# Performance work log

Hardware: AMD Instinct MI355X
Metric: run time of the kernel (lower is better)

The kernel has to match this reference:

```python
import jax, jax.numpy as jnp
import numpy as np
from jax import lax

B, C, H, W = 4, 192, 64, 64
D_STATE, D_CONV, EXPAND = 16, 4, 2.0
DI = int(EXPAND * C)           # 384 inner dim
DT_RANK = (C + 15) // 16       # 12
EPS = 1e-5


def setup_inputs() -> dict:
    key = jax.random.key(0)
    ks = jax.random.split(key, 16)
    r = lambda k, shp, s=0.02: jax.random.normal(k, shp, jnp.float32) * s
    inp = {
        'x': jax.random.normal(ks[0], (B, C, H, W), jnp.float32),
        'ln_w': jnp.ones((C,), jnp.float32),
        'ln_b': jnp.zeros((C,), jnp.float32),
        'in_proj_w': r(ks[1], (2 * DI, C)),
        'conv_w': r(ks[2], (DI, 1, D_CONV), 0.1),
        'conv_b': jnp.zeros((DI,), jnp.float32),
        'x_proj_w': r(ks[3], (DT_RANK + 2 * D_STATE, DI)),
        'dt_proj_w': r(ks[4], (DI, DT_RANK), 0.1),
        'dt_proj_b': jnp.full((DI,), -4.0, jnp.float32),  # softplus -> small dt
        'A_log': jnp.log(jnp.broadcast_to(jnp.arange(1, D_STATE + 1, dtype=jnp.float32), (DI, D_STATE))),
        'D': jnp.ones((DI,), jnp.float32),
        'out_proj_w': r(ks[5], (C, DI)),
        'rf_w': r(ks[6], (C, C, 3, 3), 0.05),
        'rf_b': jnp.zeros((C,), jnp.float32),
        'bn_w': jnp.ones((C,), jnp.float32),
        'bn_b': jnp.zeros((C,), jnp.float32),
        'bn_mean': jnp.zeros((C,), jnp.float32),
        'bn_var': jnp.ones((C,), jnp.float32),
    }
    return inp


def _selective_scan(delta, A, Bc, Cc, u):
    # delta,u: (B,L,DI); Bc,Cc: (B,L,N); A: (DI,N)
    def step(h, xs):
        d_t, b_t, c_t, u_t = xs  # (B,DI),(B,N),(B,N),(B,DI)
        dA = jnp.exp(d_t[:, :, None] * A[None])            # (B,DI,N)
        h = dA * h + (d_t * u_t)[:, :, None] * b_t[:, None, :]
        y = jnp.einsum('bdn,bn->bd', h, c_t)
        return h, y
    h0 = jnp.zeros((delta.shape[0], A.shape[0], A.shape[1]), delta.dtype)
    xs = (delta.swapaxes(0, 1), Bc.swapaxes(0, 1), Cc.swapaxes(0, 1), u.swapaxes(0, 1))
    _, ys = lax.scan(step, h0, xs)
    return ys.swapaxes(0, 1)  # (B,L,DI)


def _forward(x, ln_w, ln_b, in_proj_w, conv_w, conv_b, x_proj_w, dt_proj_w,
             dt_proj_b, A_log, D, out_proj_w, rf_w, rf_b, bn_w, bn_b, bn_mean, bn_var):
    b, c, h, w = x.shape
    L = h * w
    t = x.reshape(b, c, L).transpose(0, 2, 1)              # (B,L,C) tokens
    res = t
    mu = t.mean(-1, keepdims=True)
    var = t.var(-1, keepdims=True)
    tn = (t - mu) * lax.rsqrt(var + EPS) * ln_w + ln_b
    xz = jnp.einsum('blc,ec->ble', tn, in_proj_w)          # (B,L,2*DI)
    xi, z = jnp.split(xz, 2, axis=-1)
    # causal depthwise conv1d over L
    xi = xi.transpose(0, 2, 1)                             # (B,DI,L)
    xi = lax.conv_general_dilated(xi, conv_w, (1,), [(D_CONV - 1, 0)],
                                  feature_group_count=DI,
                                  dimension_numbers=('NCH', 'OIH', 'NCH'))
    xi = jax.nn.silu(xi + conv_b[None, :, None])
    xt = xi.transpose(0, 2, 1)                             # (B,L,DI)
    dbl = jnp.einsum('bld,ed->ble', xt, x_proj_w)
    dt, Bc, Cc = jnp.split(dbl, [DT_RANK, DT_RANK + D_STATE], axis=-1)
    delta = jax.nn.softplus(jnp.einsum('blr,dr->bld', dt, dt_proj_w) + dt_proj_b)
    A = -jnp.exp(A_log)
    y = _selective_scan(delta, A, Bc, Cc, xt) + xt * D
    y = y * jax.nn.silu(z)
    t = res + jnp.einsum('bld,cd->blc', y, out_proj_w)     # residual
    x2 = t.transpose(0, 2, 1).reshape(b, c, h, w)
    # refine: conv3x3 + BN(eval) + ReLU
    x2 = lax.conv_general_dilated(x2, rf_w, (1, 1), 'SAME',
                                  dimension_numbers=('NCHW', 'OIHW', 'NCHW'))
    x2 = x2 + rf_b[None, :, None, None]
    x2 = (x2 - bn_mean[None, :, None, None]) * lax.rsqrt(bn_var + EPS)[None, :, None, None]
    x2 = x2 * bn_w[None, :, None, None] + bn_b[None, :, None, None]
    return jax.nn.relu(x2)


def reference(x, ln_w, ln_b, in_proj_w, conv_w, conv_b, x_proj_w, dt_proj_w,
              dt_proj_b, A_log, D, out_proj_w, rf_w, rf_b, bn_w, bn_b, bn_mean, bn_var):
    return _forward(x, ln_w, ln_b, in_proj_w, conv_w, conv_b, x_proj_w, dt_proj_w,
                    dt_proj_b, A_log, D, out_proj_w, rf_w, rf_b, bn_w, bn_b,
                    bn_mean, bn_var)
```

## Files before the change

kernel.cpp:

```cpp
#include <hip/hip_runtime.h>


#define Bn 4
#define Cn 192
#define Hn 64
#define Wn 64
#define Ln 4096
#define DIn 384
#define Nst 16
#define RK 12
#define E2 768
#define NCn 64
#define EPSf 1e-5f

typedef __bf16 bf16x8 __attribute__((ext_vector_type(8)));
typedef float f32x4 __attribute__((ext_vector_type(4)));
typedef unsigned short u16;
typedef unsigned int u32;

static __device__ __forceinline__ float sigmoidf_(float v) {
    return 1.f / (1.f + __expf(-v));
}
static __device__ __forceinline__ float softplusf_(float v) {
    return v > 15.f ? v : __logf(1.f + __expf(v));
}
static __device__ __forceinline__ u16 f2bf(float f) {
    u32 u = __float_as_uint(f);
    u32 r = (u + 0x7FFFu + ((u >> 16) & 1u)) >> 16;
    return (u16)r;
}
static __device__ __forceinline__ float bf2f(u16 v) {
    return __uint_as_float(((u32)v) << 16);
}
static __device__ __forceinline__ float fexp2(float x) {
#if __has_builtin(__builtin_amdgcn_exp2f)
    return __builtin_amdgcn_exp2f(x);
#else
    return __expf(x * 0.69314718056f);
#endif
}
static __device__ __forceinline__ float quad_sum_dpp(float p) {
    float a = __int_as_float(__builtin_amdgcn_mov_dpp(__float_as_int(p), 0xB1, 0xF, 0xF, true));
    p += a;
    float b = __int_as_float(__builtin_amdgcn_mov_dpp(__float_as_int(p), 0x4E, 0xF, 0xF, true));
    return p + b;
}
static __device__ __forceinline__ void async16(const u16* g, u16* l) {
    __builtin_amdgcn_global_load_lds((__attribute__((address_space(1))) void*)g,
                                     (__attribute__((address_space(3))) void*)l, 16, 0, 0);
}

__global__ __launch_bounds__(256) void k_prep(const float* __restrict__ rfw,
                                              const float* __restrict__ xpw,
                                              const float* __restrict__ dtw,
                                              const float* __restrict__ inpw,
                                              const float* __restrict__ Wo,
                                              u16* __restrict__ wcv,
                                              u16* __restrict__ wcomb_bf,
                                              u16* __restrict__ inpw_bf,
                                              u16* __restrict__ wo_bf) {
    int g = blockIdx.x * 256 + threadIdx.x;
    if (g < 331776) {
        int tap = g / 36864;
        int rem = g - tap * 36864;
        int co = rem / Cn, ci = rem - co * Cn;
        wcv[g] = f2bf(rfw[((size_t)co * Cn + ci) * 9 + tap]);
    } else if (g < 503808) {
        int i = g - 331776;
        int row = i / 384, k = i - row * 384;
        float v = 0.f;
        if (row < 384) {
#pragma unroll
            for (int r = 0; r < RK; ++r)
                v = fmaf(dtw[row * RK + r], xpw[r * 384 + k], v);
        } else if (row < 416) {
            v = xpw[(RK + row - 384) * 384 + k];
        }
        wcomb_bf[i] = f2bf(v);
    } else if (g < 651264) {
        int i = g - 503808;
        inpw_bf[i] = f2bf(inpw[i]);
    } else if (g < 724992) {
        int i = g - 651264;
        wo_bf[i] = f2bf(Wo[i]);
    }
}

__global__ __launch_bounds__(256) void k_ln(const float* __restrict__ x,
                                            const float* __restrict__ lnw,
                                            const float* __restrict__ lnb,
                                            u16* __restrict__ tn_bf) {
    __shared__ float tile[Cn][65];
    __shared__ float red[2][4][64];
    __shared__ float mean_s[64], rstd_s[64];
    int b = blockIdx.x >> 6;
    int l0 = (blockIdx.x & 63) << 6;
    int tid = threadIdx.x;
    for (int idx = tid; idx < Cn * 64; idx += 256) {
        int c = idx >> 6, ll = idx & 63;
        tile[c][ll] = x[((size_t)(b * Cn + c) << 12) + l0 + ll];
    }
    __syncthreads();
    int ll = tid & 63, grp = tid >> 6;
    float s = 0.f, s2 = 0.f;
    for (int c = grp * 48; c < grp * 48 + 48; ++c) {
        float v = tile[c][ll];
        s += v; s2 += v * v;
    }
    red[0][grp][ll] = s; red[1][grp][ll] = s2;
    __syncthreads();
    if (tid < 64) {
        float m = red[0][0][tid] + red[0][1][tid] + red[0][2][tid] + red[0][3][tid];
        float q = red[1][0][tid] + red[1][1][tid] + red[1][2][tid] + red[1][3][tid];
        m *= (1.f / Cn);
        float var = q * (1.f / Cn) - m * m;
        mean_s[tid] = m;
        rstd_s[tid] = rsqrtf(var + EPSf);
    }
    __syncthreads();
    for (int idx = tid; idx < 64 * Cn; idx += 256) {
        int t = idx / Cn, c = idx - t * Cn;
        float v = (tile[c][t] - mean_s[t]) * rstd_s[t] * lnw[c] + lnb[c];
        tn_bf[(size_t)(b * Ln + l0 + t) * Cn + c] = f2bf(v);
    }
}

template <int K, int KT, int EPI, int NB, int LDO>
__global__ __launch_bounds__(256) void k_gemm3(const u16* __restrict__ A,
                                               const u16* __restrict__ W,
                                               const float* __restrict__ auxf,
                                               const u16* __restrict__ auxb,
                                               void* __restrict__ out1,
                                               float* __restrict__ out2) {
    __shared__ __align__(16) u16 As[2][64 * 64];
    __shared__ __align__(16) u16 Ws[2][64 * 64];
    int bid = blockIdx.x;
    int q = gridDim.x >> 3;
    int wk = (bid & 7) * q + (bid >> 3);
    int n0 = (wk % NB) << 6;
    int m0 = (wk / NB) << 6;
    int tid = threadIdx.x;
    int wid = tid >> 6, lane = tid & 63;
    int lrow = lane & 15, koct = lane >> 4;
    int sw = lrow & 7;
    int i0 = (wid << 7) + lane;
    int r0 = i0 >> 3, g0 = (i0 & 7) ^ (r0 & 7);
    int i1 = i0 + 64;
    int r1 = i1 >> 3, g1 = (i1 & 7) ^ (r1 & 7);
    const u16* a0p = A + (size_t)(m0 + r0) * K + g0 * 8;
    const u16* a1p = A + (size_t)(m0 + r1) * K + g1 * 8;
    const u16* w0p = W + (size_t)(n0 + r0) * K + g0 * 8;
    const u16* w1p = W + (size_t)(n0 + r1) * K + g1 * 8;
    int lb0 = (wid << 7) << 3;
    int lb1 = lb0 + 512;
    f32x4 acc[4];
#pragma unroll
    for (int j = 0; j < 4; ++j) acc[j] = (f32x4){0.f, 0.f, 0.f, 0.f};

    async16(a0p, &As[0][lb0]); async16(a1p, &As[0][lb1]);
    async16(w0p, &Ws[0][lb0]); async16(w1p, &Ws[0][lb1]);
    __syncthreads();
    for (int kt = 0; kt < KT; ++kt) {
        int cur = kt & 1;
        if (kt + 1 < KT) {
            int kk = (kt + 1) << 6;
            async16(a0p + kk, &As[cur ^ 1][lb0]);
            async16(a1p + kk, &As[cur ^ 1][lb1]);
            async16(w0p + kk, &Ws[cur ^ 1][lb0]);
            async16(w1p + kk, &Ws[cur ^ 1][lb1]);
        }
#pragma unroll
        for (int ks = 0; ks < 2; ++ks) {
            int p8 = (((ks << 2) + koct) ^ sw) << 3;
            bf16x8 a  = *(const bf16x8*)&As[cur][(((wid << 4) + lrow) << 6) + p8];
            bf16x8 b0 = *(const bf16x8*)&Ws[cur][(lrow << 6) + p8];
            bf16x8 b1 = *(const bf16x8*)&Ws[cur][((16 + lrow) << 6) + p8];
            bf16x8 b2 = *(const bf16x8*)&Ws[cur][((32 + lrow) << 6) + p8];
            bf16x8 b3 = *(const bf16x8*)&Ws[cur][((48 + lrow) << 6) + p8];
            acc[0] = __builtin_amdgcn_mfma_f32_16x16x32_bf16(a, b0, acc[0], 0, 0, 0);
            acc[1] = __builtin_amdgcn_mfma_f32_16x16x32_bf16(a, b1, acc[1], 0, 0, 0);
            acc[2] = __builtin_amdgcn_mfma_f32_16x16x32_bf16(a, b2, acc[2], 0, 0, 0);
            acc[3] = __builtin_amdgcn_mfma_f32_16x16x32_bf16(a, b3, acc[3], 0, 0, 0);
        }
        __syncthreads();
    }
    int mrow = m0 + (wid << 4) + (koct << 2);
#pragma unroll
    for (int nf = 0; nf < 4; ++nf) {
        int col = n0 + (nf << 4) + lrow;
        if constexpr (EPI == 0) {
            u16* o = (u16*)out1;
#pragma unroll
            for (int r = 0; r < 4; ++r)
                o[(size_t)(mrow + r) * LDO + col] = f2bf(acc[nf][r]);
        } else if constexpr (EPI == 1) {
            if (col < 384) {
                float dtbc = auxf[col];
                u32* dedux = (u32*)out1;
#pragma unroll
                for (int r = 0; r < 4; ++r) {
                    int m = mrow + r;
                    float de = softplusf_(acc[nf][r] + dtbc);
                    float u = bf2f(auxb[(size_t)m * DIn + col]);
                    dedux[(size_t)m * DIn + col] = (u32)f2bf(de) | ((u32)f2bf(de * u) << 16);
                }
            } else if (col < 416) {
#pragma unroll
                for (int r = 0; r < 4; ++r)
                    out2[(size_t)(mrow + r) * 32 + (col - 384)] = acc[nf][r];
            }
        } else {
            u16* t2 = (u16*)out1;
#pragma unroll
            for (int r = 0; r < 4; ++r) {
                int m = mrow + r;
                int b = m >> 12, l = m & 4095;
                float v = acc[nf][r] + auxf[((size_t)(b * Cn + col) << 12) + l];
                t2[(size_t)m * Cn + col] = f2bf(v);
            }
        }
    }
}

__global__ __launch_bounds__(256) void k_conv1d(const u16* __restrict__ xz,
                                                const float* __restrict__ cw,
                                                const float* __restrict__ cb,
                                                u16* __restrict__ xt_bf) {
    int g = blockIdx.x * 256 + threadIdx.x;
    int m = g / 96, dq = g - m * 96;
    int d = dq << 2;
    int l = m & (Ln - 1);
    float w_[4][4];
    *(float4*)&w_[0][0] = *(const float4*)&cw[(d + 0) << 2];
    *(float4*)&w_[1][0] = *(const float4*)&cw[(d + 1) << 2];
    *(float4*)&w_[2][0] = *(const float4*)&cw[(d + 2) << 2];
    *(float4*)&w_[3][0] = *(const float4*)&cw[(d + 3) << 2];
    float4 bv = *(const float4*)&cb[d];
    float o_[4] = {bv.x, bv.y, bv.z, bv.w};
    const u16* base = xz + (size_t)m * E2 + d;
#pragma unroll
    for (int j = 0; j < 4; ++j) {
        if (l >= j) {
            ushort4 in4 = *(const ushort4*)(base - (size_t)j * E2);
            o_[0] += bf2f(in4.x) * w_[0][3 - j];
            o_[1] += bf2f(in4.y) * w_[1][3 - j];
            o_[2] += bf2f(in4.z) * w_[2][3 - j];
            o_[3] += bf2f(in4.w) * w_[3][3 - j];
        }
    }
    ushort4 rb;
    rb.x = f2bf(o_[0] * sigmoidf_(o_[0]));
    rb.y = f2bf(o_[1] * sigmoidf_(o_[1]));
    rb.z = f2bf(o_[2] * sigmoidf_(o_[2]));
    rb.w = f2bf(o_[3] * sigmoidf_(o_[3]));
    *(ushort4*)&xt_bf[(size_t)m * DIn + d] = rb;
}

__global__ __launch_bounds__(256) void k_scan1(const u32* __restrict__ dedux,
                                               const float* __restrict__ bc,
                                               const float* __restrict__ alog,
                                               float* __restrict__ chunkA,
                                               float* __restrict__ chunkH) {
    __shared__ __align__(16) float ds_de[16][20], ds_dux[16][20], ds_bt[16][20];
    int dg = blockIdx.x, c = blockIdx.y, b = blockIdx.z;
    int tid = threadIdx.x;
    int dl = tid >> 4, n = tid & 15;
    int trow = dl, dd = n;
    float Av2 = -__expf(alog[(dg * 16 + dl) * Nst + n]) * 1.44269504f;
    float h = 0.f, sde = 0.f;
    int row0 = b * Ln + c * 64 + trow;
    u32 vN = dedux[(size_t)row0 * DIn + dg * 16 + dd];
    float bN = bc[(size_t)row0 * 32 + dd];
    for (int sub = 0; sub < 4; ++sub) {
        ds_de[dd][trow] = bf2f((u16)(vN & 0xffffu));
        ds_dux[dd][trow] = bf2f((u16)(vN >> 16));
        ds_bt[dd][trow] = bN;
        __syncthreads();
        if (sub < 3) {
            int row = row0 + (sub + 1) * 16;
            vN = dedux[(size_t)row * DIn + dg * 16 + dd];
            bN = bc[(size_t)row * 32 + dd];
        }
#pragma unroll
        for (int t4 = 0; t4 < 4; ++t4) {
            f32x4 de4 = *(const f32x4*)&ds_de[dl][t4 * 4];
            f32x4 dux4 = *(const f32x4*)&ds_dux[dl][t4 * 4];
            f32x4 bb4 = *(const f32x4*)&ds_bt[n][t4 * 4];
#pragma unroll
            for (int j = 0; j < 4; ++j) {
                float a = fexp2(de4[j] * Av2);
                sde += de4[j];
                h = fmaf(a, h, dux4[j] * bb4[j]);
            }
        }
        __syncthreads();
    }
    size_t base = (size_t)(b * NCn + c) * (DIn * Nst) + dg * 256;
    chunkA[base + tid] = fexp2(Av2 * sde);
    chunkH[base + tid] = h;
}

__global__ __launch_bounds__(256) void k_scan15(const float* __restrict__ chunkA,
                                                const float* __restrict__ chunkH,
                                                float* __restrict__ hstart) {
    int dg = blockIdx.x, b = blockIdx.y;
    int tid = threadIdx.x;
    size_t off = (size_t)b * NCn * (DIn * Nst) + dg * 256 + tid;
    float h = 0.f;
    for (int c0 = 0; c0 < NCn; c0 += 8) {
        float Ar[8], Hr[8];
#pragma unroll
        for (int j = 0; j < 8; ++j) {
            Ar[j] = chunkA[off + (size_t)(c0 + j) * (DIn * Nst)];
            Hr[j] = chunkH[off + (size_t)(c0 + j) * (DIn * Nst)];
        }
#pragma unroll
        for (int j = 0; j < 8; ++j) {
            hstart[off + (size_t)(c0 + j) * (DIn * Nst)] = h;
            h = fmaf(Ar[j], h, Hr[j]);
        }
    }
}

__global__ __launch_bounds__(256) void k_scan2(const u32* __restrict__ dedux,
                                               const float* __restrict__ bc,
                                               const float* __restrict__ alog,
                                               const float* __restrict__ hstart,
                                               const u16* __restrict__ xt_bf,
                                               const u16* __restrict__ xz,
                                               const float* __restrict__ Dp,
                                               u16* __restrict__ agate) {
    __shared__ __align__(16) float ds_de[16][20], ds_dux[16][20], ds_bt[16][20], ds_ct[16][20];
    __shared__ __align__(16) float pq[16][16][4];
    int dg = blockIdx.x, c = blockIdx.y, b = blockIdx.z;
    int tid = threadIdx.x;
    int dl = tid >> 4, n = tid & 15;
    int trow = dl, dd = n;
    int aq = n >> 2, bq = n & 3;
    float Av2 = -__expf(alog[(dg * 16 + dl) * Nst + n]) * 1.44269504f;
    float Dr = Dp[dg * 16 + dd];
    float msk[4];
#pragma unroll
    for (int j = 0; j < 4; ++j) msk[j] = (bq == j) ? 1.f : 0.f;
    size_t base = (size_t)(b * NCn + c) * (DIn * Nst) + dg * 256;
    float h = hstart[base + tid];
    int row0 = b * Ln + c * 64 + trow;
    u32 vN = dedux[(size_t)row0 * DIn + dg * 16 + dd];
    float bN = bc[(size_t)row0 * 32 + dd];
    float cN = bc[(size_t)row0 * 32 + 16 + dd];
    u16 uN = xt_bf[(size_t)row0 * DIn + dg * 16 + dd];
    u16 zN = xz[(size_t)row0 * E2 + DIn + dg * 16 + dd];
    for (int sub = 0; sub < 4; ++sub) {
        int row = row0 + sub * 16;
        size_t doff = (size_t)row * DIn + dg * 16 + dd;
        ds_de[dd][trow] = bf2f((u16)(vN & 0xffffu));
        ds_dux[dd][trow] = bf2f((u16)(vN >> 16));
        ds_bt[dd][trow] = bN;
        ds_ct[dd][trow] = cN;
        float uu = bf2f(uN), zz = bf2f(zN);
        __syncthreads();
        if (sub < 3) {
            int rown = row0 + (sub + 1) * 16;
            vN = dedux[(size_t)rown * DIn + dg * 16 + dd];
            bN = bc[(size_t)rown * 32 + dd];
            cN = bc[(size_t)rown * 32 + 16 + dd];
            uN = xt_bf[(size_t)rown * DIn + dg * 16 + dd];
            zN = xz[(size_t)rown * E2 + DIn + dg * 16 + dd];
        }
        float P[4] = {0.f, 0.f, 0.f, 0.f};
#pragma unroll
        for (int t4 = 0; t4 < 4; ++t4) {
            f32x4 de4 = *(const f32x4*)&ds_de[dl][t4 * 4];
            f32x4 dux4 = *(const f32x4*)&ds_dux[dl][t4 * 4];
            f32x4 bb4 = *(const f32x4*)&ds_bt[n][t4 * 4];
            f32x4 ct4 = *(const f32x4*)&ds_ct[n][t4 * 4];
#pragma unroll
            for (int j = 0; j < 4; ++j) {
                float a = fexp2(de4[j] * Av2);
                h = fmaf(a, h, dux4[j] * bb4[j]);
                float p = quad_sum_dpp(h * ct4[j]);
                P[t4] = fmaf(msk[j], p, P[t4]);
            }
        }
#pragma unroll
        for (int tt = 0; tt < 4; ++tt)
            pq[tt * 4 + bq][dl][aq] = P[tt];
        __syncthreads();
        f32x4 p4 = *(const f32x4*)&pq[trow][dd][0];
        float y = (p4[0] + p4[1]) + (p4[2] + p4[3]);
        float ga = (y + uu * Dr) * (zz * sigmoidf_(zz));
        agate[doff] = f2bf(ga);
    }
}

__global__ __launch_bounds__(256) void k_conv3(const u16* __restrict__ t2bf,
                                               const u16* __restrict__ wcv,
                                               const float* __restrict__ rfb,
                                               const float* __restrict__ bnw,
                                               const float* __restrict__ bnb,
                                               const float* __restrict__ bnm,
                                               const float* __restrict__ bnv,
                                               float* __restrict__ out) {
    __shared__ __align__(16) u16 in_s[4 * 66 * 40];
    __shared__ __align__(16) u16 w_s[9 * 64 * 40];
    int mt = blockIdx.x;
    int n0 = blockIdx.y << 6;
    int b = mt >> 5;
    int h0 = (mt & 31) << 1;
    int hw0 = h0 << 6;
    int tid = threadIdx.x;
    int wid = tid >> 6, lane = tid & 63;
    int lrow = lane & 15, lk8 = (lane >> 4) << 3, l4 = (lane >> 4) << 2;

    for (int idx = tid; idx < 4 * 40; idx += 256) {
        int rl = idx / 40, k = idx - rl * 40;
        in_s[(rl * 66 + 0) * 40 + k] = 0;
        in_s[(rl * 66 + 65) * 40 + k] = 0;
    }

    int s0 = wid * 32 + lrow;
    int s1 = s0 + 16;
    int abase0 = ((s0 >> 6) * 66 + (s0 & 63)) * 40 + lk8;
    int abase1 = ((s1 >> 6) * 66 + (s1 & 63)) * 40 + lk8;
    int bbase = lrow * 40 + lk8;

    f32x4 acc[2][4];
#pragma unroll
    for (int i = 0; i < 2; ++i)
#pragma unroll
        for (int j = 0; j < 4; ++j) acc[i][j] = (f32x4){0.f, 0.f, 0.f, 0.f};

    int wq = tid >> 2, cq = (tid & 3) << 3;
    uint4 rin[4], rw[9];
#pragma unroll
    for (int rl = 0; rl < 4; ++rl) {
        int gr = h0 - 1 + rl;
        rin[rl] = make_uint4(0u, 0u, 0u, 0u);
        if (gr >= 0 && gr < Hn)
            rin[rl] = *(const uint4*)&t2bf[(size_t)((b << 12) + (gr << 6) + wq) * Cn + cq];
    }
#pragma unroll
    for (int tap = 0; tap < 9; ++tap)
        rw[tap] = *(const uint4*)&wcv[((size_t)tap * Cn + n0 + wq) * Cn + cq];

    for (int ci0 = 0; ci0 < Cn; ci0 += 32) {
#pragma unroll
        for (int rl = 0; rl < 4; ++rl)
            *(uint4*)&in_s[(rl * 66 + wq + 1) * 40 + cq] = rin[rl];
#pragma unroll
        for (int tap = 0; tap < 9; ++tap)
            *(uint4*)&w_s[(tap * 64 + wq) * 40 + cq] = rw[tap];
        __syncthreads();
        if (ci0 + 32 < Cn) {
            int cin = ci0 + 32;
#pragma unroll
            for (int rl = 0; rl < 4; ++rl) {
                int gr = h0 - 1 + rl;
                rin[rl] = make_uint4(0u, 0u, 0u, 0u);
                if (gr >= 0 && gr < Hn)
                    rin[rl] = *(const uint4*)&t2bf[(size_t)((b << 12) + (gr << 6) + wq) * Cn + cin + cq];
            }
#pragma unroll
            for (int tap = 0; tap < 9; ++tap)
                rw[tap] = *(const uint4*)&wcv[((size_t)tap * Cn + n0 + wq) * Cn + cin + cq];
        }
#pragma unroll
        for (int kh = 0; kh < 3; ++kh) {
#pragma unroll
            for (int kw = 0; kw < 3; ++kw) {
                int aoff = (kh * 66 + kw) * 40;
                bf16x8 a0 = *(const bf16x8*)&in_s[abase0 + aoff];
                bf16x8 a1 = *(const bf16x8*)&in_s[abase1 + aoff];
                int boff = (kh * 3 + kw) * 2560;
#pragma unroll
                for (int nf = 0; nf < 4; ++nf) {
                    bf16x8 bb = *(const bf16x8*)&w_s[bbase + nf * 640 + boff];
                    acc[0][nf] = __builtin_amdgcn_mfma_f32_16x16x32_bf16(a0, bb, acc[0][nf], 0, 0, 0);
                    acc[1][nf] = __builtin_amdgcn_mfma_f32_16x16x32_bf16(a1, bb, acc[1][nf], 0, 0, 0);
                }
            }
        }
        __syncthreads();
    }
#pragma unroll
    for (int nf = 0; nf < 4; ++nf) {
        int co = n0 + nf * 16 + lrow;
        float sc = bnw[co] * rsqrtf(bnv[co] + EPSf);
        float sf = (rfb[co] - bnm[co]) * sc + bnb[co];
        size_t obase = ((size_t)(b * Cn + co) << 12) + hw0;
#pragma unroll
        for (int mf = 0; mf < 2; ++mf) {
            int sb = wid * 32 + mf * 16 + l4;
            float4 o;
            o.x = fmaxf(acc[mf][nf][0] * sc + sf, 0.f);
            o.y = fmaxf(acc[mf][nf][1] * sc + sf, 0.f);
            o.z = fmaxf(acc[mf][nf][2] * sc + sf, 0.f);
            o.w = fmaxf(acc[mf][nf][3] * sc + sf, 0.f);
            *(float4*)&out[obase + sb] = o;
        }
    }
}

extern "C" void kernel_launch(void* const* d_in, const int* in_sizes, int n_in,
                              void* d_out, int out_size, void* d_ws, size_t ws_size,
                              hipStream_t stream) {
    const float* x    = (const float*)d_in[0];
    const float* lnw  = (const float*)d_in[1];
    const float* lnb  = (const float*)d_in[2];
    const float* inpw = (const float*)d_in[3];
    const float* cw   = (const float*)d_in[4];
    const float* cb   = (const float*)d_in[5];
    const float* xpw  = (const float*)d_in[6];
    const float* dtw  = (const float*)d_in[7];
    const float* dtb  = (const float*)d_in[8];
    const float* alog = (const float*)d_in[9];
    const float* Dp   = (const float*)d_in[10];
    const float* Wo   = (const float*)d_in[11];
    const float* rfw  = (const float*)d_in[12];
    const float* rfb  = (const float*)d_in[13];
    const float* bnw  = (const float*)d_in[14];
    const float* bnb  = (const float*)d_in[15];
    const float* bnm  = (const float*)d_in[16];
    const float* bnv  = (const float*)d_in[17];

    float* ws = (float*)d_ws;
    u16* tn_bf    = (u16*)ws;
    u16* t2bf     = (u16*)ws;
    float* hstart = ws + 1572864;
    u16* xz       = (u16*)(ws + 3145728);
    u16* xt_bf    = (u16*)(ws + 9437184);
    u32* dedux    = (u32*)(ws + 12582912);
    float* bc     = ws + 18874368;
    u16* agate    = (u16*)(ws + 19398656);
    float* chunkA = ws + 22544384;
    float* chunkH = ws + 24117248;
    u16* wcv      = (u16*)(ws + 25690112);
    u16* wcomb_bf = (u16*)(ws + 25856000);
    u16* inpw_bf  = (u16*)(ws + 25942016);
    u16* wo_bf    = (u16*)(ws + 26015744);

    k_prep<<<2832, 256, 0, stream>>>(rfw, xpw, dtw, inpw, Wo, wcv, wcomb_bf, inpw_bf, wo_bf);
    k_ln<<<Bn * (Ln / 64), 256, 0, stream>>>(x, lnw, lnb, tn_bf);
    k_gemm3<Cn, 3, 0, 12, E2><<<(Bn * Ln / 64) * 12, 256, 0, stream>>>(
        tn_bf, inpw_bf, nullptr, nullptr, xz, nullptr);
    k_conv1d<<<(Bn * Ln * (DIn / 4)) / 256, 256, 0, stream>>>(xz, cw, cb, xt_bf);
    k_gemm3<DIn, 6, 1, 7, 0><<<(Bn * Ln / 64) * 7, 256, 0, stream>>>(
        xt_bf, wcomb_bf, dtb, xt_bf, dedux, bc);
    k_scan1<<<dim3(DIn / 16, NCn, Bn), 256, 0, stream>>>(dedux, bc, alog, chunkA, chunkH);
    k_scan15<<<dim3(DIn / 16, Bn), 256, 0, stream>>>(chunkA, chunkH, hstart);
    k_scan2<<<dim3(DIn / 16, NCn, Bn), 256, 0, stream>>>(dedux, bc, alog, hstart,
                                                         xt_bf, xz, Dp, agate);
    k_gemm3<DIn, 6, 2, 3, Cn><<<(Bn * Ln / 64) * 3, 256, 0, stream>>>(
        agate, wo_bf, x, nullptr, t2bf, nullptr);
    k_conv3<<<dim3(128, Cn / 64), 256, 0, stream>>>(t2bf, wcv, rfb, bnw, bnb, bnm, bnv,
                                                    (float*)d_out);
}
```

Baseline: 205.6 us.

## Rewrite 3x3 conv as implicit GEMM over zero-padded activations with async LDS loads

The out-projection GEMM now writes its output into a zero-padded (66x66) NHWC buffer, so the 3x3 conv needs no border handling. The conv is rewritten as an implicit GEMM: one block per image row and 64 output channels, stepping K over 27 tiles (9 taps x 3 chunks of 64). Operands are streamed with double-buffered global_load_lds into XOR-swizzled LDS, and the block index is remapped to spread work across XCDs. BN scale and shift are precomputed in the prep kernel. The cost is an extra memset of the padded buffer and smaller per-block tiles, with 4 waves each computing a single 16-row M fragment.

```diff
diff --git a/kernel.cpp b/kernel.cpp
--- a/kernel.cpp
+++ b/kernel.cpp
@@ -12,6 +12,8 @@
 #define E2 768
 #define NCn 64
 #define EPSf 1e-5f
+#define HP 66
+#define HP2 4356
 
 typedef __bf16 bf16x8 __attribute__((ext_vector_type(8)));
 typedef float f32x4 __attribute__((ext_vector_type(4)));
@@ -55,16 +57,22 @@
                                               const float* __restrict__ dtw,
                                               const float* __restrict__ inpw,
                                               const float* __restrict__ Wo,
-                                              u16* __restrict__ wcv,
+                                              const float* __restrict__ rfb,
+                                              const float* __restrict__ bnw,
+                                              const float* __restrict__ bnb,
+                                              const float* __restrict__ bnm,
+                                              const float* __restrict__ bnv,
+                                              u16* __restrict__ wcv2,
                                               u16* __restrict__ wcomb_bf,
                                               u16* __restrict__ inpw_bf,
-                                              u16* __restrict__ wo_bf) {
+                                              u16* __restrict__ wo_bf,
+                                              float* __restrict__ scsf) {
     int g = blockIdx.x * 256 + threadIdx.x;
     if (g < 331776) {
-        int tap = g / 36864;
-        int rem = g - tap * 36864;
-        int co = rem / Cn, ci = rem - co * Cn;
-        wcv[g] = f2bf(rfw[((size_t)co * Cn + ci) * 9 + tap]);
+        int co = g / 1728;
+        int rem = g - co * 1728;
+        int tap = rem / Cn, ci = rem - tap * Cn;
+        wcv2[g] = f2bf(rfw[((size_t)co * Cn + ci) * 9 + tap]);
     } else if (g < 503808) {
         int i = g - 331776;
         int row = i / 384, k = i - row * 384;
@@ -83,6 +91,15 @@
     } else if (g < 724992) {
         int i = g - 651264;
         wo_bf[i] = f2bf(Wo[i]);
+    } else if (g < 725376) {
+        int i = g - 724992;
+        if (i < 192) {
+            scsf[i] = bnw[i] * rsqrtf(bnv[i] + EPSf);
+        } else {
+            int c = i - 192;
+            float sc = bnw[c] * rsqrtf(bnv[c] + EPSf);
+            scsf[i] = (rfb[c] - bnm[c]) * sc + bnb[c];
+        }
     }
 }
 
@@ -215,8 +232,9 @@
             for (int r = 0; r < 4; ++r) {
                 int m = mrow + r;
                 int b = m >> 12, l = m & 4095;
+                int h = l >> 6, w = l & 63;
                 float v = acc[nf][r] + auxf[((size_t)(b * Cn + col) << 12) + l];
-                t2[(size_t)m * Cn + col] = f2bf(v);
+                t2[(size_t)(b * HP2 + (h + 1) * HP + (w + 1)) * Cn + col] = f2bf(v);
             }
         }
     }
@@ -393,111 +411,81 @@
     }
 }
 
-__global__ __launch_bounds__(256) void k_conv3(const u16* __restrict__ t2bf,
-                                               const u16* __restrict__ wcv,
-                                               const float* __restrict__ rfb,
-                                               const float* __restrict__ bnw,
-                                               const float* __restrict__ bnb,
-                                               const float* __restrict__ bnm,
-                                               const float* __restrict__ bnv,
-                                               float* __restrict__ out) {
-    __shared__ __align__(16) u16 in_s[4 * 66 * 40];
-    __shared__ __align__(16) u16 w_s[9 * 64 * 40];
-    int mt = blockIdx.x;
-    int n0 = blockIdx.y << 6;
-    int b = mt >> 5;
-    int h0 = (mt & 31) << 1;
-    int hw0 = h0 << 6;
+__global__ __launch_bounds__(256) void k_conv3g(const u16* __restrict__ t2pad,
+                                                const u16* __restrict__ wcv2,
+                                                const float* __restrict__ scsf,
+                                                float* __restrict__ out) {
+    __shared__ __align__(16) u16 As[2][64 * 64];
+    __shared__ __align__(16) u16 Ws[2][64 * 64];
+    int bid = blockIdx.x;
+    int q = gridDim.x >> 3;
+    int wk = (bid & 7) * q + (bid >> 3);
+    int n0 = (wk % 3) << 6;
+    int rowid = wk / 3;
+    int b = rowid >> 6, h = rowid & 63;
     int tid = threadIdx.x;
     int wid = tid >> 6, lane = tid & 63;
-    int lrow = lane & 15, lk8 = (lane >> 4) << 3, l4 = (lane >> 4) << 2;
-
-    for (int idx = tid; idx < 4 * 40; idx += 256) {
-        int rl = idx / 40, k = idx - rl * 40;
-        in_s[(rl * 66 + 0) * 40 + k] = 0;
-        in_s[(rl * 66 + 65) * 40 + k] = 0;
-    }
-
-    int s0 = wid * 32 + lrow;
-    int s1 = s0 + 16;
-    int abase0 = ((s0 >> 6) * 66 + (s0 & 63)) * 40 + lk8;
-    int abase1 = ((s1 >> 6) * 66 + (s1 & 63)) * 40 + lk8;
-    int bbase = lrow * 40 + lk8;
-
-    f32x4 acc[2][4];
-#pragma unroll
-    for (int i = 0; i < 2; ++i)
-#pragma unroll
-        for (int j = 0; j < 4; ++j) acc[i][j] = (f32x4){0.f, 0.f, 0.f, 0.f};
-
-    int wq = tid >> 2, cq = (tid & 3) << 3;
-    uint4 rin[4], rw[9];
-#pragma unroll
-    for (int rl = 0; rl < 4; ++rl) {
-        int gr = h0 - 1 + rl;
-        rin[rl] = make_uint4(0u, 0u, 0u, 0u);
-        if (gr >= 0 && gr < Hn)
-            rin[rl] = *(const uint4*)&t2bf[(size_t)((b << 12) + (gr << 6) + wq) * Cn + cq];
-    }
-#pragma unroll
-    for (int tap = 0; tap < 9; ++tap)
-        rw[tap] = *(const uint4*)&wcv[((size_t)tap * Cn + n0 + wq) * Cn + cq];
-
-    for (int ci0 = 0; ci0 < Cn; ci0 += 32) {
-#pragma unroll
-        for (int rl = 0; rl < 4; ++rl)
-            *(uint4*)&in_s[(rl * 66 + wq + 1) * 40 + cq] = rin[rl];
-#pragma unroll
-        for (int tap = 0; tap < 9; ++tap)
-            *(uint4*)&w_s[(tap * 64 + wq) * 40 + cq] = rw[tap];
+    int lrow = lane & 15, koct = lane >> 4;
+    int sw = lrow & 7;
+    int i0 = (wid << 7) + lane;
+    int r0 = i0 >> 3, g0 = (i0 & 7) ^ (r0 & 7);
+    int i1 = i0 + 64;
+    int r1 = i1 >> 3, g1 = (i1 & 7) ^ (r1 & 7);
+    const u16* Abase = t2pad + (size_t)(b * HP2 + (h + 1) * HP + 1) * Cn;
+    const u16* a0p = Abase + r0 * Cn + g0 * 8;
+    const u16* a1p = Abase + r1 * Cn + g1 * 8;
+    const u16* w0p = wcv2 + (size_t)(n0 + r0) * 1728 + g0 * 8;
+    const u16* w1p = wcv2 + (size_t)(n0 + r1) * 1728 + g1 * 8;
+    int lb0 = (wid << 7) << 3;
+    int lb1 = lb0 + 512;
+    const int tapoff[9] = {-HP - 1, -HP, -HP + 1, -1, 0, 1, HP - 1, HP, HP + 1};
+    f32x4 acc[4];
+#pragma unroll
+    for (int j = 0; j < 4; ++j) acc[j] = (f32x4){0.f, 0.f, 0.f, 0.f};
+
+    {
+        int koff = tapoff[0] * Cn;
+        async16(a0p + koff, &As[0][lb0]); async16(a1p + koff, &As[0][lb1]);
+        async16(w0p, &Ws[0][lb0]); async16(w1p, &Ws[0][lb1]);
+    }
+    __syncthreads();
+    for (int kt = 0; kt < 27; ++kt) {
+        int cur = kt & 1;
+        if (kt + 1 < 27) {
+            int t = (kt + 1) / 3;
+            int koff = tapoff[t] * Cn + (((kt + 1) - t * 3) << 6);
+            async16(a0p + koff, &As[cur ^ 1][lb0]);
+            async16(a1p + koff, &As[cur ^ 1][lb1]);
+            int kw = (kt + 1) << 6;
+            async16(w0p + kw, &Ws[cur ^ 1][lb0]);
+            async16(w1p + kw, &Ws[cur ^ 1][lb1]);
+        }
+#pragma unroll
+        for (int ks = 0; ks < 2; ++ks) {
+            int p8 = (((ks << 2) + koct) ^ sw) << 3;
+            bf16x8 a  = *(const bf16x8*)&As[cur][(((wid << 4) + lrow) << 6) + p8];
+            bf16x8 b0 = *(const bf16x8*)&Ws[cur][(lrow << 6) + p8];
+            bf16x8 b1 = *(const bf16x8*)&Ws[cur][((16 + lrow) << 6) + p8];
+            bf16x8 b2 = *(const bf16x8*)&Ws[cur][((32 + lrow) << 6) + p8];
+            bf16x8 b3 = *(const bf16x8*)&Ws[cur][((48 + lrow) << 6) + p8];
+            acc[0] = __builtin_amdgcn_mfma_f32_16x16x32_bf16(a, b0, acc[0], 0, 0, 0);
+            acc[1] = __builtin_amdgcn_mfma_f32_16x16x32_bf16(a, b1, acc[1], 0, 0, 0);
+            acc[2] = __builtin_amdgcn_mfma_f32_16x16x32_bf16(a, b2, acc[2], 0, 0, 0);
+            acc[3] = __builtin_amdgcn_mfma_f32_16x16x32_bf16(a, b3, acc[3], 0, 0, 0);
+        }
         __syncthreads();
-        if (ci0 + 32 < Cn) {
-            int cin = ci0 + 32;
-#pragma unroll
-            for (int rl = 0; rl < 4; ++rl) {
-                int gr = h0 - 1 + rl;
-                rin[rl] = make_uint4(0u, 0u, 0u, 0u);
-                if (gr >= 0 && gr < Hn)
-                    rin[rl] = *(const uint4*)&t2bf[(size_t)((b << 12) + (gr << 6) + wq) * Cn + cin + cq];
-            }
-#pragma unroll
-            for (int tap = 0; tap < 9; ++tap)
-                rw[tap] = *(const uint4*)&wcv[((size_t)tap * Cn + n0 + wq) * Cn + cin + cq];
-        }
-#pragma unroll
-        for (int kh = 0; kh < 3; ++kh) {
-#pragma unroll
-            for (int kw = 0; kw < 3; ++kw) {
-                int aoff = (kh * 66 + kw) * 40;
-                bf16x8 a0 = *(const bf16x8*)&in_s[abase0 + aoff];
-                bf16x8 a1 = *(const bf16x8*)&in_s[abase1 + aoff];
-                int boff = (kh * 3 + kw) * 2560;
-#pragma unroll
-                for (int nf = 0; nf < 4; ++nf) {
-                    bf16x8 bb = *(const bf16x8*)&w_s[bbase + nf * 640 + boff];
-                    acc[0][nf] = __builtin_amdgcn_mfma_f32_16x16x32_bf16(a0, bb, acc[0][nf], 0, 0, 0);
-                    acc[1][nf] = __builtin_amdgcn_mfma_f32_16x16x32_bf16(a1, bb, acc[1][nf], 0, 0, 0);
-                }
-            }
-        }
-        __syncthreads();
-    }
+    }
+    int w0_ = (wid << 4) + (koct << 2);
 #pragma unroll
     for (int nf = 0; nf < 4; ++nf) {
-        int co = n0 + nf * 16 + lrow;
-        float sc = bnw[co] * rsqrtf(bnv[co] + EPSf);
-        float sf = (rfb[co] - bnm[co]) * sc + bnb[co];
-        size_t obase = ((size_t)(b * Cn + co) << 12) + hw0;
-#pragma unroll
-        for (int mf = 0; mf < 2; ++mf) {
-            int sb = wid * 32 + mf * 16 + l4;
-            float4 o;
-            o.x = fmaxf(acc[mf][nf][0] * sc + sf, 0.f);
-            o.y = fmaxf(acc[mf][nf][1] * sc + sf, 0.f);
-            o.z = fmaxf(acc[mf][nf][2] * sc + sf, 0.f);
-            o.w = fmaxf(acc[mf][nf][3] * sc + sf, 0.f);
-            *(float4*)&out[obase + sb] = o;
-        }
+        int col = n0 + (nf << 4) + lrow;
+        float sc = scsf[col], sf = scsf[192 + col];
+        float4 o;
+        o.x = fmaxf(acc[nf][0] * sc + sf, 0.f);
+        o.y = fmaxf(acc[nf][1] * sc + sf, 0.f);
+        o.z = fmaxf(acc[nf][2] * sc + sf, 0.f);
+        o.w = fmaxf(acc[nf][3] * sc + sf, 0.f);
+        *(float4*)&out[((size_t)(b * Cn + col) << 12) + (h << 6) + w0_] = o;
     }
 }
 
@@ -525,7 +513,6 @@
 
     float* ws = (float*)d_ws;
     u16* tn_bf    = (u16*)ws;
-    u16* t2bf     = (u16*)ws;
     float* hstart = ws + 1572864;
     u16* xz       = (u16*)(ws + 3145728);
     u16* xt_bf    = (u16*)(ws + 9437184);
@@ -534,12 +521,16 @@
     u16* agate    = (u16*)(ws + 19398656);
     float* chunkA = ws + 22544384;
     float* chunkH = ws + 24117248;
-    u16* wcv      = (u16*)(ws + 25690112);
+    u16* wcv2     = (u16*)(ws + 25690112);
     u16* wcomb_bf = (u16*)(ws + 25856000);
     u16* inpw_bf  = (u16*)(ws + 25942016);
     u16* wo_bf    = (u16*)(ws + 26015744);
-
-    k_prep<<<2832, 256, 0, stream>>>(rfw, xpw, dtw, inpw, Wo, wcv, wcomb_bf, inpw_bf, wo_bf);
+    float* scsf   = ws + 26052608;
+    u16* t2pad    = (u16*)(ws + 26053120);
+
+    hipMemsetAsync(t2pad, 0, (size_t)Bn * HP2 * Cn * sizeof(u16), stream);
+    k_prep<<<2834, 256, 0, stream>>>(rfw, xpw, dtw, inpw, Wo, rfb, bnw, bnb, bnm, bnv,
+                                     wcv2, wcomb_bf, inpw_bf, wo_bf, scsf);
     k_ln<<<Bn * (Ln / 64), 256, 0, stream>>>(x, lnw, lnb, tn_bf);
     k_gemm3<Cn, 3, 0, 12, E2><<<(Bn * Ln / 64) * 12, 256, 0, stream>>>(
         tn_bf, inpw_bf, nullptr, nullptr, xz, nullptr);
@@ -551,7 +542,6 @@
     k_scan2<<<dim3(DIn / 16, NCn, Bn), 256, 0, stream>>>(dedux, bc, alog, hstart,
                                                          xt_bf, xz, Dp, agate);
     k_gemm3<DIn, 6, 2, 3, Cn><<<(Bn * Ln / 64) * 3, 256, 0, stream>>>(
-        agate, wo_bf, x, nullptr, t2bf, nullptr);
-    k_conv3<<<dim3(128, Cn / 64), 256, 0, stream>>>(t2bf, wcv, rfb, bnw, bnb, bnm, bnv,
-                                                    (float*)d_out);
-}
+        agate, wo_bf, x, nullptr, (void*)t2pad, nullptr);
+    k_conv3g<<<768, 256, 0, stream>>>(t2pad, wcv2, scsf, (float*)d_out);
+}
```

After: 186.4 us. 9.3% less time.
